# Kernel optimization log

Measured on AMD Instinct MI355X. Metric: run time of the kernel, lower is better.

The kernel has to match this reference:

```python
import jax, jax.numpy as jnp
import numpy as np

NUM_USER = 200000
NUM_ITEM = 200000
DIM_E = 64
DIM_FEAT = 128
B = 16384
NUM_NEG = 16
TEMP = 0.2
LR_LAMBDA = 0.5
NUM_SAMPLE = 0.5


def _l2norm(x, eps=1e-12):
    # F.normalize(x, dim=1): x / max(||x||_2, eps)
    n = jnp.sqrt(jnp.sum(x * x, axis=1, keepdims=True))
    return x / jnp.maximum(n, eps)


def setup_inputs() -> dict:
    key = jax.random.key(0)
    ks = jax.random.split(key, 9)
    G = 1 + NUM_NEG
    N = B * G
    v_feat = jax.random.normal(ks[0], (NUM_ITEM, DIM_FEAT), dtype=jnp.float32)
    id_embedding = jax.random.normal(ks[1], (NUM_USER + NUM_ITEM, DIM_E), dtype=jnp.float32) * 0.05
    W1 = jax.random.normal(ks[2], (DIM_FEAT, 256), dtype=jnp.float32) * (1.0 / np.sqrt(DIM_FEAT))
    b1 = jnp.zeros((256,), dtype=jnp.float32)
    W2 = jax.random.normal(ks[3], (256, DIM_E), dtype=jnp.float32) * (1.0 / np.sqrt(256.0))
    b2 = jnp.zeros((DIM_E,), dtype=jnp.float32)
    user_tensor = jax.random.randint(ks[4], (B, G), 0, NUM_USER, dtype=jnp.int32)
    # item ids are global ids in [num_user, num_user + num_item)
    item_tensor = jax.random.randint(ks[5], (B, G), NUM_USER, NUM_USER + NUM_ITEM, dtype=jnp.int32)
    num_to_replace = int(N * NUM_SAMPLE)
    rand_index = jax.random.randint(ks[6], (num_to_replace,), 0, N, dtype=jnp.int32)
    return {
        'v_feat': v_feat, 'id_embedding': id_embedding,
        'W1': W1, 'b1': b1, 'W2': W2, 'b2': b2,
        'user_tensor': user_tensor, 'item_tensor': item_tensor,
        'rand_index': rand_index,
    }


def _encoder(v_feat, W1, b1, W2, b2):
    vf = _l2norm(v_feat)                      # F.normalize in __init__
    h = jax.nn.leaky_relu(vf @ W1 + b1)       # negative_slope=0.01 (torch default)
    return h @ W2 + b2                        # [num_item, dim_E]


def _loss_contrastive(anchor, allv):
    # exp(<a, v>/T) reshaped to [B, 1+num_neg]; col 0 is positive
    s = jnp.exp(jnp.sum(anchor * allv, axis=1) / TEMP).reshape(-1, 1 + NUM_NEG)
    pos = s[:, 0]
    tot = jnp.sum(s, axis=1)
    return jnp.mean(-jnp.log(pos / (tot + 1e-8) + 1e-8))


def reference(v_feat, id_embedding, W1, b1, W2, b2, user_tensor, item_tensor, rand_index):
    G = 1 + NUM_NEG
    feature = _encoder(v_feat, W1, b1, W2, b2)           # [num_item, dim_E]
    pos_item = jnp.repeat(item_tensor[:, :1], G, axis=1).reshape(-1)  # [B*G]
    uflat = user_tensor.reshape(-1)
    iflat = item_tensor.reshape(-1)
    item_idx = jnp.clip(iflat - NUM_USER, 0, feature.shape[0] - 1)
    all_item_feat = feature[item_idx]                    # [B*G, dim_E]
    user_emb = id_embedding[uflat]
    pos_emb = id_embedding[pos_item]
    all_emb = id_embedding[iflat]
    head_feat = _l2norm(all_item_feat)
    head_embed = _l2norm(pos_emb)
    # replace a random subset of embedding rows with encoded features
    all_item_input = all_emb.at[rand_index].set(all_item_feat[rand_index])
    l1 = _loss_contrastive(head_embed, head_feat)
    l2 = _loss_contrastive(user_emb, all_item_input)
    return LR_LAMBDA * l1 + (1.0 - LR_LAMBDA) * l2
```

## Files before the change

kernel.cpp:

```cpp
#include <hip/hip_runtime.h>
#include <hip/hip_bf16.h>

typedef __bf16 bf16_t;
typedef __bf16 bf16x8 __attribute__((ext_vector_type(8)));
typedef __bf16 bf16x4 __attribute__((ext_vector_type(4)));
typedef float f32x4 __attribute__((ext_vector_type(4)));

#define NUM_USER 200000
#define NUM_ITEM 200000
#define DIM_E 64
#define DIM_FEAT 128
#define HID 256
#define BATCH 16384
#define GG 17
#define NN (BATCH * GG)
#define NREP 139264
#define HP 40

__global__ __launch_bounds__(256) void prep2_kernel(
    const float* __restrict__ W1, const float* __restrict__ W2,
    const int* __restrict__ rand_index,
    bf16_t* __restrict__ W1t, bf16_t* __restrict__ W2t,
    unsigned char* __restrict__ mask)
{
    const int t = blockIdx.x * 256 + threadIdx.x;
    if (t < HID * DIM_FEAT) {
        const int n = t >> 7, k = t & 127;
        W1t[t] = (bf16_t)W1[k * HID + n];
    }
    if (t < DIM_E * HID) {
        const int n = t >> 8, k = t & 255;
        W2t[t] = (bf16_t)W2[k * DIM_E + n];
    }
    if (t < NREP) mask[rand_index[t]] = 1;
}

__global__ __launch_bounds__(256, 2) void encoder3_kernel(
    const float* __restrict__ vfeat,
    const bf16_t* __restrict__ W1t, const float* __restrict__ b1v,
    const bf16_t* __restrict__ W2t, const float* __restrict__ b2v,
    float* __restrict__ feature)
{
    const int wave = threadIdx.x >> 6;
    const int lane = threadIdx.x & 63;
    const int m    = lane & 15;
    const int quad = lane >> 4;
    const int wid  = blockIdx.x * 4 + wave;

    __shared__ bf16_t hlds[4][64 * HP];

    if (wid >= 3125) return;
    const size_t row_base = (size_t)wid * 64;
    bf16_t* hw = hlds[wave];

    bf16x8 af[4][4];
#pragma unroll
    for (int s = 0; s < 4; ++s) {
        const size_t row = row_base + s * 16 + m;
        const float* rp = vfeat + row * DIM_FEAT + quad * 8;
        float4 v0[4], v1[4];
#pragma unroll
        for (int ks = 0; ks < 4; ++ks) {
            v0[ks] = *reinterpret_cast<const float4*>(rp + ks * 32);
            v1[ks] = *reinterpret_cast<const float4*>(rp + ks * 32 + 4);
        }
        float ss = 0.f;
#pragma unroll
        for (int ks = 0; ks < 4; ++ks) {
            ss += v0[ks].x * v0[ks].x + v0[ks].y * v0[ks].y
                + v0[ks].z * v0[ks].z + v0[ks].w * v0[ks].w;
            ss += v1[ks].x * v1[ks].x + v1[ks].y * v1[ks].y
                + v1[ks].z * v1[ks].z + v1[ks].w * v1[ks].w;
        }
        ss += __shfl_xor(ss, 16, 64);
        ss += __shfl_xor(ss, 32, 64);
        const float inv = 1.0f / fmaxf(sqrtf(ss), 1e-12f);
#pragma unroll
        for (int ks = 0; ks < 4; ++ks) {
            bf16x8 v;
            v[0] = (bf16_t)(v0[ks].x * inv); v[1] = (bf16_t)(v0[ks].y * inv);
            v[2] = (bf16_t)(v0[ks].z * inv); v[3] = (bf16_t)(v0[ks].w * inv);
            v[4] = (bf16_t)(v1[ks].x * inv); v[5] = (bf16_t)(v1[ks].y * inv);
            v[6] = (bf16_t)(v1[ks].z * inv); v[7] = (bf16_t)(v1[ks].w * inv);
            af[s][ks] = v;
        }
    }

    f32x4 acc2[4][4];
#pragma unroll
    for (int s = 0; s < 4; ++s)
#pragma unroll
        for (int n2 = 0; n2 < 4; ++n2) acc2[s][n2] = (f32x4){0.f, 0.f, 0.f, 0.f};

#pragma unroll
    for (int p = 0; p < 8; ++p) {
#pragma unroll
        for (int h = 0; h < 2; ++h) {
            const int nt = p * 2 + h;
            const bf16_t* bp = W1t + (nt * 16 + m) * DIM_FEAT + quad * 8;
            bf16x8 bfr[4];
#pragma unroll
            for (int ks = 0; ks < 4; ++ks)
                bfr[ks] = *reinterpret_cast<const bf16x8*>(bp + ks * 32);
            const float4 bias1 = *reinterpret_cast<const float4*>(b1v + nt * 16 + quad * 4);
#pragma unroll
            for (int s = 0; s < 4; ++s) {
                f32x4 a1 = (f32x4){0.f, 0.f, 0.f, 0.f};
#pragma unroll
                for (int ks = 0; ks < 4; ++ks)
                    a1 = __builtin_amdgcn_mfma_f32_16x16x32_bf16(bfr[ks], af[s][ks], a1, 0, 0, 0);
                bf16x4 hv4;
#pragma unroll
                for (int i = 0; i < 4; ++i) {
                    float hv = a1[i] + ((const float*)&bias1)[i];
                    hv = hv >= 0.f ? hv : 0.01f * hv;
                    hv4[i] = (bf16_t)hv;
                }
                *reinterpret_cast<bf16x4*>(hw + (s * 16 + m) * HP + h * 16 + quad * 4) = hv4;
            }
        }
        bf16x8 b2f[4];
#pragma unroll
        for (int n2 = 0; n2 < 4; ++n2)
            b2f[n2] = *reinterpret_cast<const bf16x8*>(W2t + (n2 * 16 + m) * HID + p * 32 + quad * 8);
#pragma unroll
        for (int s = 0; s < 4; ++s) {
            const bf16x8 a2 = *reinterpret_cast<const bf16x8*>(hw + (s * 16 + m) * HP + quad * 8);
#pragma unroll
            for (int n2 = 0; n2 < 4; ++n2)
                acc2[s][n2] = __builtin_amdgcn_mfma_f32_16x16x32_bf16(b2f[n2], a2, acc2[s][n2], 0, 0, 0);
        }
    }

#pragma unroll
    for (int n2 = 0; n2 < 4; ++n2) {
        const float4 bias2 = *reinterpret_cast<const float4*>(b2v + n2 * 16 + quad * 4);
#pragma unroll
        for (int s = 0; s < 4; ++s) {
            float4 o;
            o.x = acc2[s][n2][0] + bias2.x;
            o.y = acc2[s][n2][1] + bias2.y;
            o.z = acc2[s][n2][2] + bias2.z;
            o.w = acc2[s][n2][3] + bias2.w;
            *reinterpret_cast<float4*>(
                feature + (row_base + s * 16 + m) * DIM_E + n2 * 16 + quad * 4) = o;
        }
    }
}

__global__ __launch_bounds__(256) void loss_elem2_kernel(
    const float* __restrict__ feature, const float* __restrict__ id_emb,
    const int* __restrict__ user_t, const int* __restrict__ item_t,
    const unsigned char* __restrict__ mask,
    float* __restrict__ s1, float* __restrict__ s2)
{
    const int kq = threadIdx.x & 3;
    const int n  = blockIdx.x * 64 + (threadIdx.x >> 2);
    const int b  = n / GG;
    const int u   = user_t[n];
    const int it  = item_t[n];
    const int pos = item_t[b * GG];
    int fidx = it - NUM_USER;
    fidx = min(max(fidx, 0), NUM_ITEM - 1);

    const float4* fp  = reinterpret_cast<const float4*>(feature + (size_t)fidx * DIM_E) + kq * 4;
    const float4* up  = reinterpret_cast<const float4*>(id_emb + (size_t)u   * DIM_E) + kq * 4;
    const float4* pp  = reinterpret_cast<const float4*>(id_emb + (size_t)pos * DIM_E) + kq * 4;
    const float4* ap  = mask[n] ? fp
                      : reinterpret_cast<const float4*>(id_emb + (size_t)it * DIM_E) + kq * 4;

    float x = 0.f, y = 0.f, z = 0.f, w = 0.f;
#pragma unroll
    for (int j = 0; j < 4; ++j) {
        const float4 f = fp[j];
        const float4 p = pp[j];
        const float4 uu = up[j];
        const float4 a = ap[j];
        x += f.x * f.x + f.y * f.y + f.z * f.z + f.w * f.w;
        y += p.x * p.x + p.y * p.y + p.z * p.z + p.w * p.w;
        z += p.x * f.x + p.y * f.y + p.z * f.z + p.w * f.w;
        w += uu.x * a.x + uu.y * a.y + uu.z * a.z + uu.w * a.w;
    }
#pragma unroll
    for (int off = 1; off <= 2; off <<= 1) {
        x += __shfl_xor(x, off, 64);
        y += __shfl_xor(y, off, 64);
        z += __shfl_xor(z, off, 64);
        w += __shfl_xor(w, off, 64);
    }
    if (kq == 0) {
        const float dot1 = z / (fmaxf(sqrtf(x), 1e-12f) * fmaxf(sqrtf(y), 1e-12f));
        s1[n] = __expf(dot1 * 5.0f);
        s2[n] = __expf(w * 5.0f);
    }
}

__global__ __launch_bounds__(256) void loss_reduce_kernel(
    const float* __restrict__ s1, const float* __restrict__ s2,
    float* __restrict__ partials)
{
    const int b = blockIdx.x * 256 + threadIdx.x;
    float tot1 = 0.f, tot2 = 0.f, p1 = 0.f, p2 = 0.f;
#pragma unroll
    for (int g = 0; g < GG; ++g) {
        const float a1 = s1[b * GG + g];
        const float a2 = s2[b * GG + g];
        if (g == 0) { p1 = a1; p2 = a2; }
        tot1 += a1; tot2 += a2;
    }
    const float l1 = -logf(p1 / (tot1 + 1e-8f) + 1e-8f);
    const float l2 = -logf(p2 / (tot2 + 1e-8f) + 1e-8f);
    float v = 0.5f * l1 + 0.5f * l2;
#pragma unroll
    for (int off = 32; off > 0; off >>= 1) v += __shfl_xor(v, off, 64);
    __shared__ float red[4];
    const int wave = threadIdx.x >> 6, lane = threadIdx.x & 63;
    if (lane == 0) red[wave] = v;
    __syncthreads();
    if (threadIdx.x == 0) partials[blockIdx.x] = red[0] + red[1] + red[2] + red[3];
}

__global__ __launch_bounds__(64) void final_kernel(
    const float* __restrict__ partials, float* __restrict__ out)
{
    float v = partials[threadIdx.x];
#pragma unroll
    for (int off = 32; off > 0; off >>= 1) v += __shfl_xor(v, off, 64);
    if (threadIdx.x == 0) out[0] = v * (1.0f / BATCH);
}

extern "C" void kernel_launch(void* const* d_in, const int* in_sizes, int n_in,
                              void* d_out, int out_size, void* d_ws, size_t ws_size,
                              hipStream_t stream)
{
    (void)in_sizes; (void)n_in; (void)out_size; (void)ws_size;
    const float* v_feat    = (const float*)d_in[0];
    const float* id_emb    = (const float*)d_in[1];
    const float* W1        = (const float*)d_in[2];
    const float* b1        = (const float*)d_in[3];
    const float* W2        = (const float*)d_in[4];
    const float* b2        = (const float*)d_in[5];
    const int*   user_t    = (const int*)d_in[6];
    const int*   item_t    = (const int*)d_in[7];
    const int*   rand_idx  = (const int*)d_in[8];

    char* ws = (char*)d_ws;
    bf16_t*        W1t      = (bf16_t*)(ws + 0);
    bf16_t*        W2t      = (bf16_t*)(ws + 65536);
    unsigned char* mask     = (unsigned char*)(ws + 98304);
    float*         s1       = (float*)(ws + 376832);
    float*         s2       = (float*)(ws + 1490944);
    float*         partials = (float*)(ws + 2605056);
    float*         feature  = (float*)(ws + 2605312);

    hipMemsetAsync(mask, 0, NN, stream);
    prep2_kernel<<<544, 256, 0, stream>>>(W1, W2, rand_idx, W1t, W2t, mask);
    encoder3_kernel<<<782, 256, 0, stream>>>(v_feat, W1t, b1, W2t, b2, feature);
    loss_elem2_kernel<<<4352, 256, 0, stream>>>(feature, id_emb, user_t, item_t, mask, s1, s2);
    loss_reduce_kernel<<<64, 256, 0, stream>>>(s1, s2, partials);
    final_kernel<<<1, 64, 0, stream>>>(partials, (float*)d_out);
}
```

Before: 311.9 us.

## Stage W1 in LDS per block, store features in bf16, prenormalize positive embeddings

The encoder now gives each wave 16 rows, with 4 waves per block and a higher occupancy bound. W1 is streamed through a double-buffered shared-memory panel instead of being reloaded from global memory by every wave. Encoded features are written as bf16, which halves the write and gather traffic in the loss kernel. A new kernel normalizes each batch's positive embedding once, so the loss kernel stops re-gathering and re-normalizing it 17 times. The costs are bf16 rounding of the features used in both losses, an extra launch, and a block-wide barrier on every panel step.

```diff
diff --git a/kernel.cpp b/kernel.cpp
--- a/kernel.cpp
+++ b/kernel.cpp
@@ -16,6 +16,7 @@
 #define NN (BATCH * GG)
 #define NREP 139264
 #define HP 40
+#define W1P 136
 
 __global__ __launch_bounds__(256) void prep2_kernel(
     const float* __restrict__ W1, const float* __restrict__ W2,
@@ -35,121 +36,158 @@
     if (t < NREP) mask[rand_index[t]] = 1;
 }
 
-__global__ __launch_bounds__(256, 2) void encoder3_kernel(
+__global__ __launch_bounds__(256, 4) void encoder4_kernel(
     const float* __restrict__ vfeat,
     const bf16_t* __restrict__ W1t, const float* __restrict__ b1v,
     const bf16_t* __restrict__ W2t, const float* __restrict__ b2v,
-    float* __restrict__ feature)
-{
-    const int wave = threadIdx.x >> 6;
-    const int lane = threadIdx.x & 63;
+    bf16_t* __restrict__ featB)
+{
+    const int tid  = threadIdx.x;
+    const int wave = tid >> 6;
+    const int lane = tid & 63;
     const int m    = lane & 15;
     const int quad = lane >> 4;
-    const int wid  = blockIdx.x * 4 + wave;
-
-    __shared__ bf16_t hlds[4][64 * HP];
-
-    if (wid >= 3125) return;
-    const size_t row_base = (size_t)wid * 64;
-    bf16_t* hw = hlds[wave];
-
-    bf16x8 af[4][4];
-#pragma unroll
-    for (int s = 0; s < 4; ++s) {
-        const size_t row = row_base + s * 16 + m;
-        const float* rp = vfeat + row * DIM_FEAT + quad * 8;
-        float4 v0[4], v1[4];
-#pragma unroll
-        for (int ks = 0; ks < 4; ++ks) {
-            v0[ks] = *reinterpret_cast<const float4*>(rp + ks * 32);
-            v1[ks] = *reinterpret_cast<const float4*>(rp + ks * 32 + 4);
+    const int row0 = blockIdx.x * 64;
+    const int srow = row0 + wave * 16;
+
+    __shared__ bf16_t pan[2][32 * W1P];
+    __shared__ bf16_t hst[4][16 * HP];
+
+    const int sr0 = tid >> 4;
+    const int seg = tid & 15;
+    const int e0  = sr0 * DIM_FEAT + seg * 8;
+    const int d0  = sr0 * W1P + seg * 8;
+    const int e1  = e0 + 16 * DIM_FEAT;
+    const int d1  = d0 + 16 * W1P;
+
+    float4 st0 = *reinterpret_cast<const float4*>(W1t + e0);
+    float4 st1 = *reinterpret_cast<const float4*>(W1t + e1);
+
+    const float* rp = vfeat + (size_t)(srow + m) * DIM_FEAT + quad * 8;
+    float4 v0[4], v1[4];
+#pragma unroll
+    for (int ks = 0; ks < 4; ++ks) {
+        v0[ks] = *reinterpret_cast<const float4*>(rp + ks * 32);
+        v1[ks] = *reinterpret_cast<const float4*>(rp + ks * 32 + 4);
+    }
+    float ss = 0.f;
+#pragma unroll
+    for (int ks = 0; ks < 4; ++ks) {
+        ss += v0[ks].x * v0[ks].x + v0[ks].y * v0[ks].y
+            + v0[ks].z * v0[ks].z + v0[ks].w * v0[ks].w;
+        ss += v1[ks].x * v1[ks].x + v1[ks].y * v1[ks].y
+            + v1[ks].z * v1[ks].z + v1[ks].w * v1[ks].w;
+    }
+    ss += __shfl_xor(ss, 16, 64);
+    ss += __shfl_xor(ss, 32, 64);
+    const float inv = 1.0f / fmaxf(sqrtf(ss), 1e-12f);
+    bf16x8 af[4];
+#pragma unroll
+    for (int ks = 0; ks < 4; ++ks) {
+        bf16x8 v;
+        v[0] = (bf16_t)(v0[ks].x * inv); v[1] = (bf16_t)(v0[ks].y * inv);
+        v[2] = (bf16_t)(v0[ks].z * inv); v[3] = (bf16_t)(v0[ks].w * inv);
+        v[4] = (bf16_t)(v1[ks].x * inv); v[5] = (bf16_t)(v1[ks].y * inv);
+        v[6] = (bf16_t)(v1[ks].z * inv); v[7] = (bf16_t)(v1[ks].w * inv);
+        af[ks] = v;
+    }
+
+    *reinterpret_cast<float4*>(&pan[0][d0]) = st0;
+    *reinterpret_cast<float4*>(&pan[0][d1]) = st1;
+    __syncthreads();
+
+    bf16_t* hw = hst[wave];
+    f32x4 acc2[4];
+#pragma unroll
+    for (int n2 = 0; n2 < 4; ++n2) acc2[n2] = (f32x4){0.f, 0.f, 0.f, 0.f};
+
+    for (int p = 0; p < 8; ++p) {
+        const int cur = p & 1;
+        float4 nx0, nx1;
+        if (p < 7) {
+            const bf16_t* nsrc = W1t + (p + 1) * (32 * DIM_FEAT);
+            nx0 = *reinterpret_cast<const float4*>(nsrc + e0);
+            nx1 = *reinterpret_cast<const float4*>(nsrc + e1);
         }
-        float ss = 0.f;
-#pragma unroll
-        for (int ks = 0; ks < 4; ++ks) {
-            ss += v0[ks].x * v0[ks].x + v0[ks].y * v0[ks].y
-                + v0[ks].z * v0[ks].z + v0[ks].w * v0[ks].w;
-            ss += v1[ks].x * v1[ks].x + v1[ks].y * v1[ks].y
-                + v1[ks].z * v1[ks].z + v1[ks].w * v1[ks].w;
-        }
-        ss += __shfl_xor(ss, 16, 64);
-        ss += __shfl_xor(ss, 32, 64);
-        const float inv = 1.0f / fmaxf(sqrtf(ss), 1e-12f);
-#pragma unroll
-        for (int ks = 0; ks < 4; ++ks) {
-            bf16x8 v;
-            v[0] = (bf16_t)(v0[ks].x * inv); v[1] = (bf16_t)(v0[ks].y * inv);
-            v[2] = (bf16_t)(v0[ks].z * inv); v[3] = (bf16_t)(v0[ks].w * inv);
-            v[4] = (bf16_t)(v1[ks].x * inv); v[5] = (bf16_t)(v1[ks].y * inv);
-            v[6] = (bf16_t)(v1[ks].z * inv); v[7] = (bf16_t)(v1[ks].w * inv);
-            af[s][ks] = v;
-        }
-    }
-
-    f32x4 acc2[4][4];
-#pragma unroll
-    for (int s = 0; s < 4; ++s)
-#pragma unroll
-        for (int n2 = 0; n2 < 4; ++n2) acc2[s][n2] = (f32x4){0.f, 0.f, 0.f, 0.f};
-
-#pragma unroll
-    for (int p = 0; p < 8; ++p) {
 #pragma unroll
         for (int h = 0; h < 2; ++h) {
             const int nt = p * 2 + h;
-            const bf16_t* bp = W1t + (nt * 16 + m) * DIM_FEAT + quad * 8;
+            const bf16_t* bp = &pan[cur][(h * 16 + m) * W1P + quad * 8];
             bf16x8 bfr[4];
 #pragma unroll
             for (int ks = 0; ks < 4; ++ks)
                 bfr[ks] = *reinterpret_cast<const bf16x8*>(bp + ks * 32);
             const float4 bias1 = *reinterpret_cast<const float4*>(b1v + nt * 16 + quad * 4);
-#pragma unroll
-            for (int s = 0; s < 4; ++s) {
-                f32x4 a1 = (f32x4){0.f, 0.f, 0.f, 0.f};
-#pragma unroll
-                for (int ks = 0; ks < 4; ++ks)
-                    a1 = __builtin_amdgcn_mfma_f32_16x16x32_bf16(bfr[ks], af[s][ks], a1, 0, 0, 0);
-                bf16x4 hv4;
-#pragma unroll
-                for (int i = 0; i < 4; ++i) {
-                    float hv = a1[i] + ((const float*)&bias1)[i];
-                    hv = hv >= 0.f ? hv : 0.01f * hv;
-                    hv4[i] = (bf16_t)hv;
-                }
-                *reinterpret_cast<bf16x4*>(hw + (s * 16 + m) * HP + h * 16 + quad * 4) = hv4;
+            f32x4 a1 = (f32x4){0.f, 0.f, 0.f, 0.f};
+#pragma unroll
+            for (int ks = 0; ks < 4; ++ks)
+                a1 = __builtin_amdgcn_mfma_f32_16x16x32_bf16(bfr[ks], af[ks], a1, 0, 0, 0);
+            bf16x4 hv4;
+#pragma unroll
+            for (int i = 0; i < 4; ++i) {
+                float hv = a1[i] + ((const float*)&bias1)[i];
+                hv = hv >= 0.f ? hv : 0.01f * hv;
+                hv4[i] = (bf16_t)hv;
             }
+            *reinterpret_cast<bf16x4*>(hw + m * HP + h * 16 + quad * 4) = hv4;
         }
         bf16x8 b2f[4];
 #pragma unroll
         for (int n2 = 0; n2 < 4; ++n2)
             b2f[n2] = *reinterpret_cast<const bf16x8*>(W2t + (n2 * 16 + m) * HID + p * 32 + quad * 8);
-#pragma unroll
-        for (int s = 0; s < 4; ++s) {
-            const bf16x8 a2 = *reinterpret_cast<const bf16x8*>(hw + (s * 16 + m) * HP + quad * 8);
-#pragma unroll
-            for (int n2 = 0; n2 < 4; ++n2)
-                acc2[s][n2] = __builtin_amdgcn_mfma_f32_16x16x32_bf16(b2f[n2], a2, acc2[s][n2], 0, 0, 0);
+        const bf16x8 a2 = *reinterpret_cast<const bf16x8*>(hw + m * HP + quad * 8);
+#pragma unroll
+        for (int n2 = 0; n2 < 4; ++n2)
+            acc2[n2] = __builtin_amdgcn_mfma_f32_16x16x32_bf16(b2f[n2], a2, acc2[n2], 0, 0, 0);
+        if (p < 7) {
+            *reinterpret_cast<float4*>(&pan[cur ^ 1][d0]) = nx0;
+            *reinterpret_cast<float4*>(&pan[cur ^ 1][d1]) = nx1;
         }
+        __syncthreads();
     }
 
 #pragma unroll
     for (int n2 = 0; n2 < 4; ++n2) {
         const float4 bias2 = *reinterpret_cast<const float4*>(b2v + n2 * 16 + quad * 4);
-#pragma unroll
-        for (int s = 0; s < 4; ++s) {
-            float4 o;
-            o.x = acc2[s][n2][0] + bias2.x;
-            o.y = acc2[s][n2][1] + bias2.y;
-            o.z = acc2[s][n2][2] + bias2.z;
-            o.w = acc2[s][n2][3] + bias2.w;
-            *reinterpret_cast<float4*>(
-                feature + (row_base + s * 16 + m) * DIM_E + n2 * 16 + quad * 4) = o;
-        }
-    }
-}
-
-__global__ __launch_bounds__(256) void loss_elem2_kernel(
-    const float* __restrict__ feature, const float* __restrict__ id_emb,
+        bf16x4 o;
+        o[0] = (bf16_t)(acc2[n2][0] + bias2.x);
+        o[1] = (bf16_t)(acc2[n2][1] + bias2.y);
+        o[2] = (bf16_t)(acc2[n2][2] + bias2.z);
+        o[3] = (bf16_t)(acc2[n2][3] + bias2.w);
+        *reinterpret_cast<bf16x4*>(featB + (size_t)(srow + m) * DIM_E + n2 * 16 + quad * 4) = o;
+    }
+}
+
+__global__ __launch_bounds__(256) void pnorm_kernel(
+    const float* __restrict__ id_emb, const int* __restrict__ item_t,
+    float* __restrict__ pnrm)
+{
+    const int kq = threadIdx.x & 3;
+    const int r  = blockIdx.x * 64 + (threadIdx.x >> 2);
+    const int pos = item_t[r * GG];
+    const float4* pp = reinterpret_cast<const float4*>(id_emb + (size_t)pos * DIM_E) + kq * 4;
+    float4 v[4];
+    float ss = 0.f;
+#pragma unroll
+    for (int j = 0; j < 4; ++j) {
+        v[j] = pp[j];
+        ss += v[j].x * v[j].x + v[j].y * v[j].y + v[j].z * v[j].z + v[j].w * v[j].w;
+    }
+    ss += __shfl_xor(ss, 1, 64);
+    ss += __shfl_xor(ss, 2, 64);
+    const float inv = 1.0f / fmaxf(sqrtf(ss), 1e-12f);
+    float4* op = reinterpret_cast<float4*>(pnrm + (size_t)r * DIM_E) + kq * 4;
+#pragma unroll
+    for (int j = 0; j < 4; ++j) {
+        float4 o;
+        o.x = v[j].x * inv; o.y = v[j].y * inv; o.z = v[j].z * inv; o.w = v[j].w * inv;
+        op[j] = o;
+    }
+}
+
+__global__ __launch_bounds__(256) void loss_elem3_kernel(
+    const bf16_t* __restrict__ featB, const float* __restrict__ id_emb,
+    const float* __restrict__ pnrm,
     const int* __restrict__ user_t, const int* __restrict__ item_t,
     const unsigned char* __restrict__ mask,
     float* __restrict__ s1, float* __restrict__ s2)
@@ -157,39 +195,45 @@
     const int kq = threadIdx.x & 3;
     const int n  = blockIdx.x * 64 + (threadIdx.x >> 2);
     const int b  = n / GG;
-    const int u   = user_t[n];
-    const int it  = item_t[n];
-    const int pos = item_t[b * GG];
+    const int u  = user_t[n];
+    const int it = item_t[n];
     int fidx = it - NUM_USER;
     fidx = min(max(fidx, 0), NUM_ITEM - 1);
-
-    const float4* fp  = reinterpret_cast<const float4*>(feature + (size_t)fidx * DIM_E) + kq * 4;
-    const float4* up  = reinterpret_cast<const float4*>(id_emb + (size_t)u   * DIM_E) + kq * 4;
-    const float4* pp  = reinterpret_cast<const float4*>(id_emb + (size_t)pos * DIM_E) + kq * 4;
-    const float4* ap  = mask[n] ? fp
-                      : reinterpret_cast<const float4*>(id_emb + (size_t)it * DIM_E) + kq * 4;
-
-    float x = 0.f, y = 0.f, z = 0.f, w = 0.f;
+    const bool rep = mask[n] != 0;
+
+    const bf16x8* fp = reinterpret_cast<const bf16x8*>(featB + (size_t)fidx * DIM_E + kq * 16);
+    const float4* ph = reinterpret_cast<const float4*>(pnrm + (size_t)b * DIM_E) + kq * 4;
+    const float4* up = reinterpret_cast<const float4*>(id_emb + (size_t)u * DIM_E) + kq * 4;
+    const float4* ip = reinterpret_cast<const float4*>(id_emb + (size_t)it * DIM_E) + kq * 4;
+
+    float f[16];
+#pragma unroll
+    for (int h = 0; h < 2; ++h) {
+        const bf16x8 fv = fp[h];
+#pragma unroll
+        for (int j = 0; j < 8; ++j) f[h * 8 + j] = (float)fv[j];
+    }
+
+    float x = 0.f, z = 0.f, w = 0.f;
 #pragma unroll
     for (int j = 0; j < 4; ++j) {
-        const float4 f = fp[j];
-        const float4 p = pp[j];
+        const float4 p = ph[j];
         const float4 uu = up[j];
-        const float4 a = ap[j];
-        x += f.x * f.x + f.y * f.y + f.z * f.z + f.w * f.w;
-        y += p.x * p.x + p.y * p.y + p.z * p.z + p.w * p.w;
-        z += p.x * f.x + p.y * f.y + p.z * f.z + p.w * f.w;
-        w += uu.x * a.x + uu.y * a.y + uu.z * a.z + uu.w * a.w;
+        float4 a;
+        if (rep) { a.x = f[j*4]; a.y = f[j*4+1]; a.z = f[j*4+2]; a.w = f[j*4+3]; }
+        else     { a = ip[j]; }
+        x += f[j*4]*f[j*4] + f[j*4+1]*f[j*4+1] + f[j*4+2]*f[j*4+2] + f[j*4+3]*f[j*4+3];
+        z += p.x*f[j*4] + p.y*f[j*4+1] + p.z*f[j*4+2] + p.w*f[j*4+3];
+        w += uu.x*a.x + uu.y*a.y + uu.z*a.z + uu.w*a.w;
     }
 #pragma unroll
     for (int off = 1; off <= 2; off <<= 1) {
         x += __shfl_xor(x, off, 64);
-        y += __shfl_xor(y, off, 64);
         z += __shfl_xor(z, off, 64);
         w += __shfl_xor(w, off, 64);
     }
     if (kq == 0) {
-        const float dot1 = z / (fmaxf(sqrtf(x), 1e-12f) * fmaxf(sqrtf(y), 1e-12f));
+        const float dot1 = z / fmaxf(sqrtf(x), 1e-12f);
         s1[n] = __expf(dot1 * 5.0f);
         s2[n] = __expf(w * 5.0f);
     }
@@ -251,12 +295,14 @@
     float*         s1       = (float*)(ws + 376832);
     float*         s2       = (float*)(ws + 1490944);
     float*         partials = (float*)(ws + 2605056);
-    float*         feature  = (float*)(ws + 2605312);
+    float*         pnrm     = (float*)(ws + 2605312);
+    bf16_t*        featB    = (bf16_t*)(ws + 6799616);
 
     hipMemsetAsync(mask, 0, NN, stream);
     prep2_kernel<<<544, 256, 0, stream>>>(W1, W2, rand_idx, W1t, W2t, mask);
-    encoder3_kernel<<<782, 256, 0, stream>>>(v_feat, W1t, b1, W2t, b2, feature);
-    loss_elem2_kernel<<<4352, 256, 0, stream>>>(feature, id_emb, user_t, item_t, mask, s1, s2);
+    encoder4_kernel<<<3125, 256, 0, stream>>>(v_feat, W1t, b1, W2t, b2, featB);
+    pnorm_kernel<<<256, 256, 0, stream>>>(id_emb, item_t, pnrm);
+    loss_elem3_kernel<<<4352, 256, 0, stream>>>(featB, id_emb, pnrm, user_t, item_t, mask, s1, s2);
     loss_reduce_kernel<<<64, 256, 0, stream>>>(s1, s2, partials);
     final_kernel<<<1, 64, 0, stream>>>(partials, (float*)d_out);
 }
```

After: 321.6 us. +3.1%, slower.
